# Performance work log

Hardware: AMD Instinct MI355X
Metric: run time of the kernel (lower is better)

The kernel has to match this reference:

```python
import jax, jax.numpy as jnp
import numpy as np

H = 1024   # HIDDEN_DIM
V = 15000  # VOCAB_SIZE
L = 2      # NUM_LAYERS
E = 4      # experts per block
B, S = 32, 2048


def rmsnorm(x, w, eps=1e-6):
    return x * jax.lax.rsqrt(jnp.mean(x * x, axis=-1, keepdims=True) + eps) * w


def setup_inputs() -> dict:
    key = jax.random.key(0)
    ks = jax.random.split(key, 8)
    windows = jax.random.randint(ks[0], (B, S), 0, V, dtype=jnp.int32)
    hemis = jax.random.randint(ks[1], (B,), 0, 2, dtype=jnp.int32)
    experts = jax.random.randint(ks[2], (B,), 0, E, dtype=jnp.int32)
    emb = jax.random.normal(ks[3], (V, H), dtype=jnp.float32) * 0.02
    norm1_w = jnp.ones((L, H), dtype=jnp.float32)
    decay_logit = jnp.full((L, H), 2.0, dtype=jnp.float32)  # torch init: ones*2.0
    norm2_w = jnp.ones((L, H), dtype=jnp.float32)
    # expert weights, torch Linear layout [out, in] per expert: [L, E, H, H]
    Wexp = jax.random.normal(ks[4], (L, E, H, H), dtype=jnp.float32) * 0.02
    final_norm_w = jnp.ones((H,), dtype=jnp.float32)
    lm_head = jax.random.normal(ks[5], (V, H), dtype=jnp.float32) * 0.02
    return dict(windows=windows, hemis=hemis, experts=experts, emb=emb,
                norm1_w=norm1_w, decay_logit=decay_logit, norm2_w=norm2_w,
                Wexp=Wexp, final_norm_w=final_norm_w, lm_head=lm_head)


def reference(windows, hemis, experts, emb, norm1_w, decay_logit, norm2_w,
              Wexp, final_norm_w, lm_head):
    del hemis  # only used for router loss when targets are given (inference path)
    x = emb[windows]  # [B,S,H]
    onehot = jax.nn.one_hot(experts, E, dtype=x.dtype)  # [B,E]
    for l in range(L):
        xn = rmsnorm(x, norm1_w[l])
        decay = jax.nn.sigmoid(decay_logit[l])  # [H]

        def step(state, xt):
            s = state * decay + xt * (1.0 - decay)
            return s, s

        init = jnp.zeros((x.shape[0], H), dtype=x.dtype)
        _, states = jax.lax.scan(step, init, jnp.swapaxes(xn, 0, 1))  # [S,B,H]
        x = x + jnp.swapaxes(states, 0, 1)
        pool = rmsnorm(x, norm2_w[l])[:, -1, :]  # [B,H]
        # all 4 expert FFNs on the pooled state, then select by expert id
        out_all = jax.nn.relu(jnp.einsum('bh,edh->ebd', pool, Wexp[l]))  # [E,B,H]
        out = jnp.einsum('be,ebh->bh', onehot, out_all)  # [B,H]
        x = x + out[:, None, :]
    final_state = rmsnorm(x[:, -1, :], final_norm_w)
    logits = final_state @ lm_head.T  # [B,V]
    return logits
```

## Files before the change

### kernel.cpp

```cpp
#include <hip/hip_runtime.h>
#include <cstddef>
#include <cstdint>

#define H 1024
#define V 15000
#define NE 4
#define B 32
#define S 2048
#define EPS 1e-6f
#define CH 32
#define T0 64
#define SB 8
#define NVB 469
#define LGRID 1024

typedef unsigned short u16;

__device__ __forceinline__ float wave_sum(float x) {
#pragma unroll
  for (int off = 32; off > 0; off >>= 1) x += __shfl_down(x, off);
  return x;
}

__device__ __forceinline__ float bf2f(u16 u) {
  union { uint32_t i; float f; } x;
  x.i = ((uint32_t)u) << 16;
  return x.f;
}

__device__ __forceinline__ float bflo(uint32_t u) {
  union { uint32_t i; float f; } x;
  x.i = u << 16;
  return x.f;
}
__device__ __forceinline__ float bfhi(uint32_t u) {
  union { uint32_t i; float f; } x;
  x.i = u & 0xFFFF0000u;
  return x.f;
}

__device__ __forceinline__ u16 f2bf(float f) {
  union { float f; uint32_t i; } x;
  x.f = f;
  const uint32_t u = x.i;
  return (u16)((u + 0x7FFFu + ((u >> 16) & 1u)) >> 16);
}

__device__ __forceinline__ void pin4(float4& v) {
  asm volatile("" : "+v"(v.x), "+v"(v.y), "+v"(v.z), "+v"(v.w));
}

__global__ __launch_bounds__(256) void k_vocab(const float* __restrict__ emb,
                                               float* __restrict__ invr1,
                                               u16* __restrict__ embh) {
  const int gw = (blockIdx.x * blockDim.x + threadIdx.x) >> 6;
  const int lane = threadIdx.x & 63;
  if (gw >= V) return;
  const float4* row = (const float4*)(emb + (size_t)gw * H);
  float s = 0.f;
#pragma unroll
  for (int j = 0; j < 4; ++j) {
    const float4 f = row[lane + 64 * j];
    s += f.x * f.x + f.y * f.y + f.z * f.z + f.w * f.w;
    if (embh) {
      ushort4 h4;
      h4.x = f2bf(f.x); h4.y = f2bf(f.y); h4.z = f2bf(f.z); h4.w = f2bf(f.w);
      ((ushort4*)(embh + (size_t)gw * H))[lane + 64 * j] = h4;
    }
  }
  s = wave_sum(s);
  if (lane == 0) invr1[gw] = rsqrtf(s * (1.f / H) + EPS);
}

__global__ void k_bucket(const int* __restrict__ experts,
                         int* __restrict__ elist, int* __restrict__ ecnt) {
  if (threadIdx.x == 0 && blockIdx.x == 0) {
    int c[NE] = {0, 0, 0, 0};
    for (int b = 0; b < B; ++b) {
      const int e = experts[b];
      elist[e * B + c[e]] = b;
      c[e]++;
    }
    for (int e = 0; e < NE; ++e) ecnt[e] = c[e];
  }
}

template <int BF>
__global__ __launch_bounds__(512, 8) void k_scanA(
    const int* __restrict__ windows, const float* __restrict__ emb,
    const u16* __restrict__ embh, const float* __restrict__ norm1_w,
    const float* __restrict__ decay_logit, const float* __restrict__ invr1,
    float* __restrict__ local1) {
  __shared__ int tok_l[T0];
  __shared__ float iv_l[T0];
  const int b = blockIdx.x / CH, c = blockIdx.x % CH;
  const int tid = threadIdx.x;
  const int h2 = tid * 2;
  if (tid < T0) {
    const int tok = windows[b * S + c * T0 + tid];
    tok_l[tid] = tok << 10;
    iv_l[tid] = invr1[tok];
  }
  const float d1a = 1.f / (1.f + expf(-decay_logit[h2]));
  const float d1b = 1.f / (1.f + expf(-decay_logit[h2 + 1]));
  const float g1a = norm1_w[h2] * (1.f - d1a);
  const float g1b = norm1_w[h2 + 1] * (1.f - d1b);
  __syncthreads();
  float sa = 0.f, sbv = 0.f;
  for (int t0 = 0; t0 < T0; t0 += SB) {
    uint32_t u[SB];
    float2 ef[SB];
#pragma unroll
    for (int k = 0; k < SB; ++k) {
      if constexpr (BF)
        u[k] = *(const uint32_t*)(embh + (size_t)(tok_l[t0 + k] + h2));
      else
        ef[k] = *(const float2*)(emb + (size_t)(tok_l[t0 + k] + h2));
    }
#pragma unroll
    for (int k = 0; k < SB; ++k) {
      const float iv = iv_l[t0 + k];
      const float ea = BF ? bflo(u[k]) : ef[k].x;
      const float eb = BF ? bfhi(u[k]) : ef[k].y;
      sa = sa * d1a + ea * (iv * g1a);
      sbv = sbv * d1b + eb * (iv * g1b);
    }
  }
  *(float2*)(local1 + (size_t)(b * CH + c) * H + h2) = make_float2(sa, sbv);
}

__global__ __launch_bounds__(1024) void k_scanB(
    const int* __restrict__ windows, const float* __restrict__ emb,
    const float* __restrict__ decay_logit, const float* __restrict__ local1,
    float* __restrict__ s1start, float* __restrict__ es1,
    float* __restrict__ invp) {
  __shared__ float red[16];
  const int b = blockIdx.x, h = threadIdx.x;
  const float d1 = 1.f / (1.f + expf(-decay_logit[h]));
  float dT = d1;
#pragma unroll
  for (int i = 0; i < 6; ++i) dT *= dT;
  float Sv = 0.f;
  for (int c = 0; c < CH; ++c) {
    const size_t idx = (size_t)(b * CH + c) * H + h;
    s1start[idx] = Sv;
    Sv = dT * Sv + local1[idx];
  }
  const int tl = windows[b * S + S - 1];
  const float v = emb[(size_t)tl * H + h] + Sv;
  es1[b * H + h] = v;
  const float q = wave_sum(v * v);
  if ((h & 63) == 0) red[h >> 6] = q;
  __syncthreads();
  if (h == 0) {
    float t = 0.f;
#pragma unroll
    for (int i = 0; i < 16; ++i) t += red[i];
    invp[b] = rsqrtf(t * (1.f / H) + EPS);
  }
}

__global__ __launch_bounds__(256) void k_expert2(
    const float* __restrict__ src, const float* __restrict__ invp,
    const float* __restrict__ n2w, const float* __restrict__ Wl,
    const int* __restrict__ elist, const int* __restrict__ ecnt,
    float* __restrict__ outp) {
  const int e = blockIdx.x >> 6;
  const int dgrp = blockIdx.x & 63;
  const int cnt = ecnt[e];
  if (cnt == 0) return;
  const int wave = threadIdx.x >> 6, lane = threadIdx.x & 63;
  const float* W = Wl + (size_t)e * H * H;
  const float4* n2w4 = (const float4*)n2w;
#pragma unroll 1
  for (int i = 0; i < 4; ++i) {
    const int dd = dgrp * 16 + wave * 4 + i;
    const float4* wr4 = (const float4*)(W + (size_t)dd * H);
    float4 w4[4];
#pragma unroll
    for (int j = 0; j < 4; ++j) w4[j] = wr4[lane + 64 * j];
#pragma unroll 1
    for (int bi = 0; bi < cnt; ++bi) {
      const int b = elist[e * B + bi];
      const float4* s4 = (const float4*)(src + b * H);
      float s = 0.f;
#pragma unroll
      for (int j = 0; j < 4; ++j) {
        const float4 sv = s4[lane + 64 * j];
        const float4 nv = n2w4[lane + 64 * j];
        s += w4[j].x * sv.x * nv.x + w4[j].y * sv.y * nv.y +
             w4[j].z * sv.z * nv.z + w4[j].w * sv.w * nv.w;
      }
      s = wave_sum(s);
      if (lane == 0) outp[b * H + dd] = fmaxf(s * invp[b], 0.f);
    }
  }
}

template <int BF>
__global__ __launch_bounds__(512, 8) void k_fuseCD(
    const int* __restrict__ windows, const float* __restrict__ emb,
    const u16* __restrict__ embh, const float* __restrict__ norm1_w,
    const float* __restrict__ decay_logit, const float* __restrict__ invr1,
    const float* __restrict__ s1start, const float* __restrict__ out1,
    float* __restrict__ local2, float* __restrict__ x1last) {
  __shared__ int tok_l[T0];
  __shared__ float iv_l[T0];
  __shared__ float sq[SB][512];
  __shared__ float rinv_l[SB];
  const int b = blockIdx.x / CH, c = blockIdx.x % CH;
  const int tid = threadIdx.x;
  const int h2 = 2 * tid;
  if (tid < T0) {
    const int tok = windows[b * S + c * T0 + tid];
    tok_l[tid] = tok << 10;
    iv_l[tid] = invr1[tok];
  }
  const float d1a = 1.f / (1.f + expf(-decay_logit[h2]));
  const float d1b = 1.f / (1.f + expf(-decay_logit[h2 + 1]));
  const float g1a = norm1_w[h2] * (1.f - d1a);
  const float g1b = norm1_w[h2 + 1] * (1.f - d1b);
  const float d2a = 1.f / (1.f + expf(-decay_logit[H + h2]));
  const float d2b = 1.f / (1.f + expf(-decay_logit[H + h2 + 1]));
  const float g2a = norm1_w[H + h2] * (1.f - d2a);
  const float g2b = norm1_w[H + h2 + 1] * (1.f - d2b);
  const float2 o1 = *(const float2*)(out1 + b * H + h2);
  const float2 s1v = *(const float2*)(s1start + (size_t)(b * CH + c) * H + h2);
  float s1a = s1v.x, s1b = s1v.y;
  float s2a = 0.f, s2b = 0.f;
  __syncthreads();
  const int wv = tid >> 6, lane = tid & 63;
  float x1a[SB], x1b[SB];
  for (int sb = 0; sb < T0 / SB; ++sb) {
    uint32_t u[SB];
    float2 ef[SB];
#pragma unroll
    for (int k = 0; k < SB; ++k) {
      const int t = sb * SB + k;
      if constexpr (BF)
        u[k] = *(const uint32_t*)(embh + (size_t)(tok_l[t] + h2));
      else
        ef[k] = *(const float2*)(emb + (size_t)(tok_l[t] + h2));
    }
#pragma unroll
    for (int k = 0; k < SB; ++k) {
      const float iv = iv_l[sb * SB + k];
      const float ea = BF ? bflo(u[k]) : ef[k].x;
      const float eb = BF ? bfhi(u[k]) : ef[k].y;
      s1a = s1a * d1a + ea * (iv * g1a);
      s1b = s1b * d1b + eb * (iv * g1b);
      x1a[k] = ea + s1a + o1.x;
      x1b[k] = eb + s1b + o1.y;
      sq[k][tid] = x1a[k] * x1a[k] + x1b[k] * x1b[k];
    }
    __syncthreads();
    float ssum = 0.f;
#pragma unroll
    for (int j = 0; j < 8; ++j) ssum += sq[wv][lane + 64 * j];
    ssum = wave_sum(ssum);
    if (lane == 0) rinv_l[wv] = rsqrtf(ssum * (1.f / H) + EPS);
    __syncthreads();
#pragma unroll
    for (int k = 0; k < SB; ++k) {
      const float ra = rinv_l[k];
      s2a = s2a * d2a + x1a[k] * (ra * g2a);
      s2b = s2b * d2b + x1b[k] * (ra * g2b);
    }
  }
  *(float2*)(local2 + (size_t)(b * CH + c) * H + h2) = make_float2(s2a, s2b);
  if (c == CH - 1)
    *(float2*)(x1last + b * H + h2) = make_float2(x1a[SB - 1], x1b[SB - 1]);
}

__global__ __launch_bounds__(1024) void k_scanE(
    const float* __restrict__ decay_logit, const float* __restrict__ local2,
    const float* __restrict__ x1last, float* __restrict__ es2,
    float* __restrict__ invp) {
  __shared__ float red[16];
  const int b = blockIdx.x, h = threadIdx.x;
  const float d2 = 1.f / (1.f + expf(-decay_logit[H + h]));
  float dT = d2;
#pragma unroll
  for (int i = 0; i < 6; ++i) dT *= dT;
  float Sv = 0.f;
  for (int c = 0; c < CH; ++c)
    Sv = dT * Sv + local2[(size_t)(b * CH + c) * H + h];
  const float v = x1last[b * H + h] + Sv;
  es2[b * H + h] = v;
  const float q = wave_sum(v * v);
  if ((h & 63) == 0) red[h >> 6] = q;
  __syncthreads();
  if (h == 0) {
    float t = 0.f;
#pragma unroll
    for (int i = 0; i < 16; ++i) t += red[i];
    invp[32 + b] = rsqrtf(t * (1.f / H) + EPS);
  }
}

__global__ __launch_bounds__(256) void k_fstate(const float* __restrict__ es2,
    const float* __restrict__ out2, const float* __restrict__ fnw,
    float* __restrict__ fst) {
  __shared__ float red[4];
  const int b = blockIdx.x, tid = threadIdx.x;
  float4 x = ((const float4*)(es2 + b * H))[tid];
  const float4 y = ((const float4*)(out2 + b * H))[tid];
  x.x += y.x; x.y += y.y; x.z += y.z; x.w += y.w;
  float s = x.x * x.x + x.y * x.y + x.z * x.z + x.w * x.w;
  s = wave_sum(s);
  if ((tid & 63) == 0) red[tid >> 6] = s;
  __syncthreads();
  const float ir =
      rsqrtf((red[0] + red[1] + red[2] + red[3]) * (1.f / H) + EPS);
  const float4 w = ((const float4*)fnw)[tid];
  float4 o;
  o.x = x.x * ir * w.x; o.y = x.y * ir * w.y;
  o.z = x.z * ir * w.z; o.w = x.w * ir * w.w;
  ((float4*)(fst + b * H))[tid] = o;
}

__global__ __launch_bounds__(256, 4) void k_logits(const float* __restrict__ fst,
    const float* __restrict__ lm, float* __restrict__ part) {
  __shared__ float4 fs4[16 * 128];
  const int hh = blockIdx.x & 1;
  const int bgrp = (blockIdx.x >> 1) & 1;
  const int pblk = blockIdx.x >> 2;
  const int tid = threadIdx.x;
  const int wave = tid >> 6, lane = tid & 63;
  const int sg = lane >> 4;
  const int c = lane & 15;
  for (int j = tid; j < 16 * 128; j += 256) {
    const int bb = j >> 7, q = j & 127;
    fs4[j] = ((const float4*)fst)[(bgrp * 16 + bb) * 256 + hh * 128 + q];
  }
  __syncthreads();
  float* pdst = part + (size_t)hh * B * V + (size_t)bgrp * 16 * V;
#pragma unroll 1
  for (int vblk = pblk; vblk < NVB; vblk += LGRID / 4) {
    const int v0 = vblk * 32 + wave * 8 + sg * 2;
    float4 rv[2][8];
#pragma unroll
    for (int i = 0; i < 2; ++i) {
      int r = v0 + i;
      if (r > V - 1) r = V - 1;
      const float4* rp = (const float4*)(lm + (size_t)r * H) + hh * 128 + c;
#pragma unroll
      for (int jj = 0; jj < 8; ++jj) rv[i][jj] = rp[16 * jj];
    }
#pragma unroll
    for (int i = 0; i < 2; ++i)
#pragma unroll
      for (int jj = 0; jj < 8; ++jj) pin4(rv[i][jj]);
    float acc[2][16];
#pragma unroll
    for (int i = 0; i < 2; ++i)
#pragma unroll
      for (int bb = 0; bb < 16; ++bb) acc[i][bb] = 0.f;
#pragma unroll
    for (int jj = 0; jj < 8; ++jj) {
      const int hoff = c + 16 * jj;
#pragma unroll
      for (int bb = 0; bb < 16; ++bb) {
        const float4 fv = fs4[bb * 128 + hoff];
#pragma unroll
        for (int i = 0; i < 2; ++i) {
          acc[i][bb] += rv[i][jj].x * fv.x + rv[i][jj].y * fv.y +
                        rv[i][jj].z * fv.z + rv[i][jj].w * fv.w;
        }
      }
    }
#pragma unroll
    for (int off = 1; off < 16; off <<= 1)
#pragma unroll
      for (int i = 0; i < 2; ++i)
#pragma unroll
        for (int bb = 0; bb < 16; ++bb)
          acc[i][bb] += __shfl_xor(acc[i][bb], off);
    if (c == 0) {
#pragma unroll
      for (int bb = 0; bb < 16; ++bb)
#pragma unroll
        for (int i = 0; i < 2; ++i) {
          const int r = v0 + i;
          if (r < V) pdst[(size_t)bb * V + r] = acc[i][bb];
        }
    }
  }
}

__global__ __launch_bounds__(256) void k_comb(const float* __restrict__ part,
                                              float* __restrict__ outp) {
  const int i = blockIdx.x * 256 + threadIdx.x;
  if (i < B * V) outp[i] = part[i] + part[B * V + i];
}

extern "C" void kernel_launch(void* const* d_in, const int* in_sizes, int n_in,
                              void* d_out, int out_size, void* d_ws,
                              size_t ws_size, hipStream_t stream) {
  const int* windows = (const int*)d_in[0];
  const int* experts = (const int*)d_in[2];
  const float* emb = (const float*)d_in[3];
  const float* norm1_w = (const float*)d_in[4];
  const float* decay_logit = (const float*)d_in[5];
  const float* norm2_w = (const float*)d_in[6];
  const float* Wexp = (const float*)d_in[7];
  const float* final_norm_w = (const float*)d_in[8];
  const float* lm_head = (const float*)d_in[9];
  float* outp = (float*)d_out;

  float* ws = (float*)d_ws;
  float* invr1 = ws;
  float* local1 = invr1 + 15360;
  float* s1start = local1 + B * CH * H;
  float* local2 = s1start + B * CH * H;
  float* out1 = local2 + B * CH * H;
  float* out2 = out1 + B * H;
  float* es1 = out2 + B * H;
  float* es2 = es1 + B * H;
  float* x1last = es2 + B * H;
  float* fst = x1last + B * H;
  float* invp = fst + B * H;
  int* elist = (int*)(invp + 64);
  int* ecnt = elist + NE * B;
  float* part = local1;
  u16* embh = (u16*)(((uintptr_t)(ecnt + NE) + 255) & ~(uintptr_t)255);
  const size_t need = (size_t)((char*)embh - (char*)d_ws) + (size_t)V * H * 2;
  const bool use_bf = ws_size >= need;

  k_vocab<<<(V * 64 + 255) / 256, 256, 0, stream>>>(emb, invr1,
                                                    use_bf ? embh : nullptr);
  k_bucket<<<1, 64, 0, stream>>>(experts, elist, ecnt);
  if (use_bf)
    k_scanA<1><<<B * CH, 512, 0, stream>>>(windows, emb, embh, norm1_w,
                                           decay_logit, invr1, local1);
  else
    k_scanA<0><<<B * CH, 512, 0, stream>>>(windows, emb, embh, norm1_w,
                                           decay_logit, invr1, local1);
  k_scanB<<<B, 1024, 0, stream>>>(windows, emb, decay_logit, local1, s1start,
                                  es1, invp);
  k_expert2<<<NE * 64, 256, 0, stream>>>(es1, invp, norm2_w, Wexp, elist,
                                         ecnt, out1);
  if (use_bf)
    k_fuseCD<1><<<B * CH, 512, 0, stream>>>(windows, emb, embh, norm1_w,
                                            decay_logit, invr1, s1start,
                                            out1, local2, x1last);
  else
    k_fuseCD<0><<<B * CH, 512, 0, stream>>>(windows, emb, embh, norm1_w,
                                            decay_logit, invr1, s1start,
                                            out1, local2, x1last);
  k_scanE<<<B, 1024, 0, stream>>>(decay_logit, local2, x1last, es2, invp);
  k_expert2<<<NE * 64, 256, 0, stream>>>(es2, invp + 32, norm2_w + H,
                                         Wexp + (size_t)NE * H * H, elist,
                                         ecnt, out2);
  k_fstate<<<B, 256, 0, stream>>>(es2, out2, final_norm_w, fst);
  k_logits<<<LGRID, 256, 0, stream>>>(fst, lm_head, part);
  k_comb<<<(B * V + 255) / 256, 256, 0, stream>>>(part, outp);
}
```

Before: 302.2 us.

## Compute LM head logits with split-bf16 MFMA and drop partial-sum combine kernel

Rewrites the final logits GEMV-like product to use bf16 MFMA 16x16x32 instructions. To keep close to fp32 accuracy, both the final state and the lm_head rows are split into bf16 hi/lo parts, and three MFMAs (hh, hl, lh) are issued per tile. Each block covers 16 vocab rows and reduces the K split across its waves in shared memory, then writes the logits directly, so the two-way partial buffer and the k_comb launch go away. The kernel remains bound by reading lm_head in fp32. The hi/lo split adds ALU work, and dropping the lo*lo term adds a small amount of error.

```diff
diff --git a/kernel.cpp b/kernel.cpp
--- a/kernel.cpp
+++ b/kernel.cpp
@@ -11,10 +11,11 @@
 #define CH 32
 #define T0 64
 #define SB 8
-#define NVB 469
-#define LGRID 1024
+#define NVT 938
 
 typedef unsigned short u16;
+typedef __attribute__((ext_vector_type(8))) short bf16x8;
+typedef __attribute__((ext_vector_type(4))) float f32x4;
 
 __device__ __forceinline__ float wave_sum(float x) {
 #pragma unroll
@@ -46,8 +47,24 @@
   return (u16)((u + 0x7FFFu + ((u >> 16) & 1u)) >> 16);
 }
 
-__device__ __forceinline__ void pin4(float4& v) {
-  asm volatile("" : "+v"(v.x), "+v"(v.y), "+v"(v.z), "+v"(v.w));
+__device__ __forceinline__ float uasf(uint32_t u) {
+  union { uint32_t i; float f; } x;
+  x.i = u;
+  return x.f;
+}
+__device__ __forceinline__ uint32_t fasu(float f) {
+  union { float f; uint32_t i; } x;
+  x.f = f;
+  return x.i;
+}
+
+__device__ __forceinline__ void split2(float x0, float x1, uint32_t& hp,
+                                       uint32_t& lp) {
+  const uint32_t u0 = fasu(x0), u1 = fasu(x1);
+  hp = (u0 >> 16) | (u1 & 0xFFFF0000u);
+  const float l0 = x0 - uasf(u0 & 0xFFFF0000u);
+  const float l1 = x1 - uasf(u1 & 0xFFFF0000u);
+  asm("v_cvt_pk_bf16_f32 %0, %1, %2" : "=v"(lp) : "v"(l0), "v"(l1));
 }
 
 __global__ __launch_bounds__(256) void k_vocab(const float* __restrict__ emb,
@@ -300,7 +317,7 @@
 
 __global__ __launch_bounds__(256) void k_fstate(const float* __restrict__ es2,
     const float* __restrict__ out2, const float* __restrict__ fnw,
-    float* __restrict__ fst) {
+    u16* __restrict__ fsth, u16* __restrict__ fstl) {
   __shared__ float red[4];
   const int b = blockIdx.x, tid = threadIdx.x;
   float4 x = ((const float4*)(es2 + b * H))[tid];
@@ -313,85 +330,78 @@
   const float ir =
       rsqrtf((red[0] + red[1] + red[2] + red[3]) * (1.f / H) + EPS);
   const float4 w = ((const float4*)fnw)[tid];
-  float4 o;
-  o.x = x.x * ir * w.x; o.y = x.y * ir * w.y;
-  o.z = x.z * ir * w.z; o.w = x.w * ir * w.w;
-  ((float4*)(fst + b * H))[tid] = o;
-}
-
-__global__ __launch_bounds__(256, 4) void k_logits(const float* __restrict__ fst,
-    const float* __restrict__ lm, float* __restrict__ part) {
-  __shared__ float4 fs4[16 * 128];
-  const int hh = blockIdx.x & 1;
-  const int bgrp = (blockIdx.x >> 1) & 1;
-  const int pblk = blockIdx.x >> 2;
+  float o[4];
+  o[0] = x.x * ir * w.x; o[1] = x.y * ir * w.y;
+  o[2] = x.z * ir * w.z; o[3] = x.w * ir * w.w;
+  ushort4 hs, ls;
+  u16* hp = (u16*)&hs;
+  u16* lp = (u16*)&ls;
+#pragma unroll
+  for (int j = 0; j < 4; ++j) {
+    const uint32_t u = fasu(o[j]);
+    hp[j] = (u16)(u >> 16);
+    lp[j] = f2bf(o[j] - uasf(u & 0xFFFF0000u));
+  }
+  ((ushort4*)(fsth + b * H))[tid] = hs;
+  ((ushort4*)(fstl + b * H))[tid] = ls;
+}
+
+__global__ __launch_bounds__(256) void k_logits(const float* __restrict__ lm,
+    const u16* __restrict__ fsth, const u16* __restrict__ fstl,
+    float* __restrict__ outp) {
+  __shared__ float red[4][2][4][64];
   const int tid = threadIdx.x;
-  const int wave = tid >> 6, lane = tid & 63;
-  const int sg = lane >> 4;
-  const int c = lane & 15;
-  for (int j = tid; j < 16 * 128; j += 256) {
-    const int bb = j >> 7, q = j & 127;
-    fs4[j] = ((const float4*)fst)[(bgrp * 16 + bb) * 256 + hh * 128 + q];
-  }
-  __syncthreads();
-  float* pdst = part + (size_t)hh * B * V + (size_t)bgrp * 16 * V;
+  const int w = tid >> 6, l = tid & 63;
+  const int ln = l & 15, kg = l >> 4;
+  const int v0 = blockIdx.x * 16;
+  int r = v0 + ln;
+  if (r > V - 1) r = V - 1;
+  const int kbase = w * 256 + kg * 8;
+  const float* lrow = lm + (size_t)r * H + kbase;
+  const u16* fh0 = fsth + (size_t)ln * H + kbase;
+  const u16* fh1 = fsth + (size_t)(16 + ln) * H + kbase;
+  const u16* fl0 = fstl + (size_t)ln * H + kbase;
+  const u16* fl1 = fstl + (size_t)(16 + ln) * H + kbase;
+  f32x4 acc0 = {0.f, 0.f, 0.f, 0.f};
+  f32x4 acc1 = {0.f, 0.f, 0.f, 0.f};
 #pragma unroll 1
-  for (int vblk = pblk; vblk < NVB; vblk += LGRID / 4) {
-    const int v0 = vblk * 32 + wave * 8 + sg * 2;
-    float4 rv[2][8];
-#pragma unroll
-    for (int i = 0; i < 2; ++i) {
-      int r = v0 + i;
-      if (r > V - 1) r = V - 1;
-      const float4* rp = (const float4*)(lm + (size_t)r * H) + hh * 128 + c;
-#pragma unroll
-      for (int jj = 0; jj < 8; ++jj) rv[i][jj] = rp[16 * jj];
-    }
-#pragma unroll
-    for (int i = 0; i < 2; ++i)
-#pragma unroll
-      for (int jj = 0; jj < 8; ++jj) pin4(rv[i][jj]);
-    float acc[2][16];
-#pragma unroll
-    for (int i = 0; i < 2; ++i)
-#pragma unroll
-      for (int bb = 0; bb < 16; ++bb) acc[i][bb] = 0.f;
-#pragma unroll
-    for (int jj = 0; jj < 8; ++jj) {
-      const int hoff = c + 16 * jj;
-#pragma unroll
-      for (int bb = 0; bb < 16; ++bb) {
-        const float4 fv = fs4[bb * 128 + hoff];
-#pragma unroll
-        for (int i = 0; i < 2; ++i) {
-          acc[i][bb] += rv[i][jj].x * fv.x + rv[i][jj].y * fv.y +
-                        rv[i][jj].z * fv.z + rv[i][jj].w * fv.w;
-        }
-      }
-    }
-#pragma unroll
-    for (int off = 1; off < 16; off <<= 1)
-#pragma unroll
-      for (int i = 0; i < 2; ++i)
-#pragma unroll
-        for (int bb = 0; bb < 16; ++bb)
-          acc[i][bb] += __shfl_xor(acc[i][bb], off);
-    if (c == 0) {
-#pragma unroll
-      for (int bb = 0; bb < 16; ++bb)
-#pragma unroll
-        for (int i = 0; i < 2; ++i) {
-          const int r = v0 + i;
-          if (r < V) pdst[(size_t)bb * V + r] = acc[i][bb];
-        }
-    }
-  }
-}
-
-__global__ __launch_bounds__(256) void k_comb(const float* __restrict__ part,
-                                              float* __restrict__ outp) {
-  const int i = blockIdx.x * 256 + threadIdx.x;
-  if (i < B * V) outp[i] = part[i] + part[B * V + i];
+  for (int it = 0; it < 8; ++it) {
+    const int ko = it * 32;
+    const float4 xa = *(const float4*)(lrow + ko);
+    const float4 xb = *(const float4*)(lrow + ko + 4);
+    union { bf16x8 v; uint32_t u[4]; } Bh, Bl, Ah0, Ah1, Al0, Al1;
+    split2(xa.x, xa.y, Bh.u[0], Bl.u[0]);
+    split2(xa.z, xa.w, Bh.u[1], Bl.u[1]);
+    split2(xb.x, xb.y, Bh.u[2], Bl.u[2]);
+    split2(xb.z, xb.w, Bh.u[3], Bl.u[3]);
+    *(uint4*)Ah0.u = *(const uint4*)(fh0 + ko);
+    *(uint4*)Ah1.u = *(const uint4*)(fh1 + ko);
+    *(uint4*)Al0.u = *(const uint4*)(fl0 + ko);
+    *(uint4*)Al1.u = *(const uint4*)(fl1 + ko);
+    acc0 = __builtin_amdgcn_mfma_f32_16x16x32_bf16(Ah0.v, Bh.v, acc0, 0, 0, 0);
+    acc1 = __builtin_amdgcn_mfma_f32_16x16x32_bf16(Ah1.v, Bh.v, acc1, 0, 0, 0);
+    acc0 = __builtin_amdgcn_mfma_f32_16x16x32_bf16(Ah0.v, Bl.v, acc0, 0, 0, 0);
+    acc1 = __builtin_amdgcn_mfma_f32_16x16x32_bf16(Ah1.v, Bl.v, acc1, 0, 0, 0);
+    acc0 = __builtin_amdgcn_mfma_f32_16x16x32_bf16(Al0.v, Bh.v, acc0, 0, 0, 0);
+    acc1 = __builtin_amdgcn_mfma_f32_16x16x32_bf16(Al1.v, Bh.v, acc1, 0, 0, 0);
+  }
+#pragma unroll
+  for (int q = 0; q < 4; ++q) {
+    red[w][0][q][l] = acc0[q];
+    red[w][1][q][l] = acc1[q];
+  }
+  __syncthreads();
+  const int rr = tid >> 6, lane2 = tid & 63;
+  const int vv = v0 + (lane2 & 15);
+  if (vv < V) {
+#pragma unroll
+    for (int mt = 0; mt < 2; ++mt) {
+      const float s = red[0][mt][rr][lane2] + red[1][mt][rr][lane2] +
+                      red[2][mt][rr][lane2] + red[3][mt][rr][lane2];
+      const int bb = mt * 16 + 4 * (lane2 >> 4) + rr;
+      outp[(size_t)bb * V + vv] = s;
+    }
+  }
 }
 
 extern "C" void kernel_launch(void* const* d_in, const int* in_sizes, int n_in,
@@ -418,12 +428,12 @@
   float* es1 = out2 + B * H;
   float* es2 = es1 + B * H;
   float* x1last = es2 + B * H;
-  float* fst = x1last + B * H;
-  float* invp = fst + B * H;
+  float* invp = x1last + B * H;
   int* elist = (int*)(invp + 64);
   int* ecnt = elist + NE * B;
-  float* part = local1;
-  u16* embh = (u16*)(((uintptr_t)(ecnt + NE) + 255) & ~(uintptr_t)255);
+  u16* fsth = (u16*)(ecnt + NE);
+  u16* fstl = fsth + B * H;
+  u16* embh = (u16*)(((uintptr_t)(fstl + B * H) + 255) & ~(uintptr_t)255);
   const size_t need = (size_t)((char*)embh - (char*)d_ws) + (size_t)V * H * 2;
   const bool use_bf = ws_size >= need;
 
@@ -452,7 +462,6 @@
   k_expert2<<<NE * 64, 256, 0, stream>>>(es2, invp + 32, norm2_w + H,
                                          Wexp + (size_t)NE * H * H, elist,
                                          ecnt, out2);
-  k_fstate<<<B, 256, 0, stream>>>(es2, out2, final_norm_w, fst);
-  k_logits<<<LGRID, 256, 0, stream>>>(fst, lm_head, part);
-  k_comb<<<(B * V + 255) / 256, 256, 0, stream>>>(part, outp);
-}
+  k_fstate<<<B, 256, 0, stream>>>(es2, out2, final_norm_w, fsth, fstl);
+  k_logits<<<NVT, 256, 0, stream>>>(lm_head, fsth, fstl, outp);
+}
```

After: 303.0 us. About the same (+0.2%).
